# Kernel optimization log

Hardware: AMD Instinct MI355X
Metric: run time of the kernel (lower is better)

## Reference

```python
import jax, jax.numpy as jnp
import numpy as np

D_STATE = 16
D_CONV = 4
DT_RANK = 2  # ceil(d_model/16) with d_model=32


def _conv2d(x, w, b, pad, dil=1, groups=1):
    y = jax.lax.conv_general_dilated(
        x, w, (1, 1), ((pad, pad), (pad, pad)), rhs_dilation=(dil, dil),
        feature_group_count=groups, dimension_numbers=('NCHW', 'OIHW', 'NCHW'))
    return y + b[None, :, None, None]


def _ssm(xc, delta, A, Bc, Cc, D):
    # xc,delta: (B,L,Di); A: (Di,N); Bc,Cc: (B,L,N)
    dA = jnp.exp(delta[..., None] * A)                       # (B,L,Di,N)
    dBx = delta[..., None] * Bc[:, :, None, :] * xc[..., None]
    def comb(e1, e2):
        a1, b1 = e1
        a2, b2 = e2
        return a2 * a1, a2 * b1 + b2
    _, h = jax.lax.associative_scan(comb, (dA, dBx), axis=1)  # h_t = dA_t*h_{t-1}+dBx_t
    return jnp.einsum('bldn,bln->bld', h, Cc) + xc * D


def _dir(xin, cw, cb, wx, wdt, bdt, A_log, D):
    # causal depthwise conv1d over L, then silu
    L = xin.shape[1]
    xp = jnp.pad(xin, ((0, 0), (D_CONV - 1, 0), (0, 0)))
    xc = sum(xp[:, k:k + L, :] * cw[:, k] for k in range(D_CONV)) + cb
    xc = jax.nn.silu(xc)
    dbc = xc @ wx.T                                          # (B,L,dt_rank+2N)
    dt, Bc, Cc = jnp.split(dbc, [DT_RANK, DT_RANK + D_STATE], axis=-1)
    delta = jax.nn.softplus(dt @ wdt.T + bdt)
    return _ssm(xc, delta, -jnp.exp(A_log), Bc, Cc, D)


def _mamba(xn, w_in, cwf, cbf, wxf, wdtf, bdtf, Af, Df,
           cwb, cbb, wxb, wdtb, bdtb, Ab, Db, w_out):
    xz = xn @ w_in.T                                         # (B,L,2*Di)
    xin, z = jnp.split(xz, 2, axis=-1)
    y_f = _dir(xin, cwf, cbf, wxf, wdtf, bdtf, Af, Df)
    y_b = jnp.flip(_dir(jnp.flip(xin, axis=1), cwb, cbb, wxb, wdtb, bdtb, Ab, Db), axis=1)
    return ((y_f + y_b) * jax.nn.silu(z)) @ w_out.T          # bimamba v2: sum of directions


def _forward(x, w_att, b_att, ln_w, ln_b, w_in,
             conv_w_f, conv_b_f, wx_f, wdt_f, bdt_f, A_log_f, D_f,
             conv_w_b, conv_b_b, wx_b, wdt_b, bdt_b, A_log_b, D_b,
             w_out, w_se, b_se, w_conv, b_conv):
    B, C, H, W = x.shape
    att1 = x
    xa = _conv2d(x, w_att, b_att, pad=9, dil=3, groups=C)    # dilated depthwise, same HxW
    xf = xa.reshape(B, C, H * W).transpose(0, 2, 1)          # (B,L,C)
    mu = xf.mean(-1, keepdims=True)
    var = xf.var(-1, keepdims=True)
    xn = (xf - mu) / jnp.sqrt(var + 1e-5) * ln_w + ln_b
    out = _mamba(xn, w_in, conv_w_f, conv_b_f, wx_f, wdt_f, bdt_f, A_log_f, D_f,
                 conv_w_b, conv_b_b, wx_b, wdt_b, bdt_b, A_log_b, D_b, w_out)
    att2 = out.transpose(0, 2, 1).reshape(B, C, H, W)
    att = jnp.concatenate([att1, att2], axis=1)
    pooled = jnp.concatenate([att.mean(1, keepdims=True), att.max(1, keepdims=True)], axis=1)
    se = jax.nn.sigmoid(_conv2d(pooled, w_se, b_se, pad=3))
    output = att1 * se[:, 0:1] + att2 * se[:, 1:2]
    return _conv2d(output, w_conv, b_conv, pad=1)


def setup_inputs() -> dict:
    key = jax.random.key(0)
    ks = jax.random.split(key, 16)
    B, C, H, W = 4, 32, 96, 96
    Di, OUT = 64, 64
    n = jax.random.normal
    A_log = jnp.tile(jnp.log(jnp.arange(1, D_STATE + 1, dtype=jnp.float32)), (Di, 1))
    return {
        'x': n(ks[0], (B, C, H, W), jnp.float32),
        'w_att': n(ks[1], (C, 1, 7, 7), jnp.float32) * 0.05,
        'b_att': jnp.zeros((C,), jnp.float32),
        'ln_w': jnp.ones((C,), jnp.float32),
        'ln_b': jnp.zeros((C,), jnp.float32),
        'w_in': n(ks[2], (2 * Di, C), jnp.float32) / np.sqrt(C),
        'conv_w_f': n(ks[3], (Di, D_CONV), jnp.float32) * 0.3,
        'conv_b_f': jnp.zeros((Di,), jnp.float32),
        'wx_f': n(ks[4], (DT_RANK + 2 * D_STATE, Di), jnp.float32) / np.sqrt(Di),
        'wdt_f': n(ks[5], (Di, DT_RANK), jnp.float32) * 0.5,
        'bdt_f': n(ks[6], (Di,), jnp.float32) * 0.1,
        'A_log_f': A_log,
        'D_f': jnp.ones((Di,), jnp.float32),
        'conv_w_b': n(ks[7], (Di, D_CONV), jnp.float32) * 0.3,
        'conv_b_b': jnp.zeros((Di,), jnp.float32),
        'wx_b': n(ks[8], (DT_RANK + 2 * D_STATE, Di), jnp.float32) / np.sqrt(Di),
        'wdt_b': n(ks[9], (Di, DT_RANK), jnp.float32) * 0.5,
        'bdt_b': n(ks[10], (Di,), jnp.float32) * 0.1,
        'A_log_b': A_log,
        'D_b': jnp.ones((Di,), jnp.float32),
        'w_out': n(ks[11], (C, Di), jnp.float32) / np.sqrt(Di),
        'w_se': n(ks[12], (2, 2, 7, 7), jnp.float32) * 0.1,
        'b_se': jnp.zeros((2,), jnp.float32),
        'w_conv': n(ks[13], (OUT, C, 3, 3), jnp.float32) * 0.06,
        'b_conv': jnp.zeros((OUT,), jnp.float32),
    }


def reference(x, w_att, b_att, ln_w, ln_b, w_in,
              conv_w_f, conv_b_f, wx_f, wdt_f, bdt_f, A_log_f, D_f,
              conv_w_b, conv_b_b, wx_b, wdt_b, bdt_b, A_log_b, D_b,
              w_out, w_se, b_se, w_conv, b_conv):
    return _forward(x, w_att, b_att, ln_w, ln_b, w_in,
                    conv_w_f, conv_b_f, wx_f, wdt_f, bdt_f, A_log_f, D_f,
                    conv_w_b, conv_b_b, wx_b, wdt_b, bdt_b, A_log_b, D_b,
                    w_out, w_se, b_se, w_conv, b_conv)
```

## Files before the change

### kernel.cpp

```cpp
#include <hip/hip_runtime.h>
#include <math.h>

#define BB 4
#define CH 32
#define HH 96
#define WW 96
#define LL (HH*WW)
#define DI 64
#define NS 16
#define BL (BB*LL)
#define NCH 144
#define CLEN (LL/NCH)
#define GG 8

__device__ __forceinline__ float sigmoidf_(float x){ return 1.f/(1.f+__expf(-x)); }
__device__ __forceinline__ float siluf_(float x){ return x*sigmoidf_(x); }
__device__ __forceinline__ float softplusf_(float x){
  return (x > 15.f) ? x : __logf(1.f + __expf(x));
}
#define WAVE_LDS_FENCE() do { asm volatile("s_waitcnt lgkmcnt(0)" ::: "memory"); __builtin_amdgcn_sched_barrier(0); } while(0)

__global__ __launch_bounds__(256) void k1_conv_att(
    const float* __restrict__ x, const float* __restrict__ w,
    const float* __restrict__ bias, float* __restrict__ xa){
  int idx = blockIdx.x*256 + threadIdx.x;
  if (idx >= BB*CH*LL) return;
  int w0 = idx % WW; int h0 = (idx/WW) % HH; int c = (idx/LL) % CH;
  const float* xp = x + (idx/LL)*LL;
  const float* wp = w + c*49;
  float acc = bias[c];
  #pragma unroll
  for (int kh=0; kh<7; ++kh){
    int hh = h0 + 3*kh - 9;
    if ((unsigned)hh >= HH) continue;
    const float* row = xp + hh*WW;
    #pragma unroll
    for (int kw=0; kw<7; ++kw){
      int ww = w0 + 3*kw - 9;
      if ((unsigned)ww < WW) acc += row[ww]*wp[kh*7+kw];
    }
  }
  xa[idx] = acc;
}

__global__ __launch_bounds__(128) void k2_ln_inproj(
    const float* __restrict__ xa, const float* __restrict__ w_in,
    const float* __restrict__ ln_w, const float* __restrict__ ln_b,
    float* __restrict__ xin, float* __restrict__ zs){
  __shared__ float xs[CH*68];
  __shared__ float smu[64], srs[64];
  int tid = threadIdx.x;
  int tg0 = blockIdx.x*64;
  int bb = tg0 / LL;
  int l0 = tg0 % LL;
  const float* xab = xa + bb*CH*LL + l0;
  for (int r=0; r<16; ++r){
    int idx = r*128 + tid;
    int c = idx >> 6, t = idx & 63;
    xs[c*68+t] = xab[c*LL + t];
  }
  int j = tid;
  float wlj[CH];
  float swl=0.f, bj=0.f;
  #pragma unroll
  for (int c=0;c<CH;++c){
    float wv = ln_w[c]*w_in[j*CH+c];
    wlj[c] = wv; swl += wv;
    bj += ln_b[c]*w_in[j*CH+c];
  }
  __syncthreads();
  if (tid < 64){
    float s=0.f, s2=0.f;
    #pragma unroll
    for (int c=0;c<CH;++c){ float v = xs[c*68+tid]; s+=v; s2+=v*v; }
    float mu = s*(1.f/CH);
    float var = s2*(1.f/CH) - mu*mu;
    smu[tid]=mu; srs[tid]=rsqrtf(var+1e-5f);
  }
  __syncthreads();
  for (int t4=0;t4<16;++t4){
    float a0=0.f,a1=0.f,a2=0.f,a3=0.f;
    #pragma unroll
    for (int c=0;c<CH;++c){
      float4 xv = *(const float4*)&xs[c*68 + t4*4];
      float wv = wlj[c];
      a0 += xv.x*wv; a1 += xv.y*wv; a2 += xv.z*wv; a3 += xv.w*wv;
    }
    float av[4] = {a0,a1,a2,a3};
    #pragma unroll
    for (int q=0;q<4;++q){
      int t = t4*4+q;
      float out = srs[t]*(av[q] - smu[t]*swl) + bj;
      int base = ((bb*LL) + l0 + t)*DI;
      if (j < DI) xin[base + j] = out;
      else        zs[base + (j-DI)] = siluf_(out);
    }
  }
}

__global__ __launch_bounds__(64) void k3_fused(
    const float* __restrict__ xin,
    const float* __restrict__ cw_f, const float* __restrict__ cb_f,
    const float* __restrict__ wx_f, const float* __restrict__ wdt_f, const float* __restrict__ bdt_f,
    const float* __restrict__ Al_f,
    const float* __restrict__ cw_b, const float* __restrict__ cb_b,
    const float* __restrict__ wx_b, const float* __restrict__ wdt_b, const float* __restrict__ bdt_b,
    const float* __restrict__ Al_b,
    float* __restrict__ xc_f, float* __restrict__ dl_f, float* __restrict__ Bc_f, float* __restrict__ Cc_f,
    float* __restrict__ xc_b, float* __restrict__ dl_b, float* __restrict__ Bc_b, float* __restrict__ Cc_b,
    float* __restrict__ aggP, float* __restrict__ aggS){
  int lane = threadIdx.x;
  int dir = blockIdx.y;
  int bb = blockIdx.z;
  int ch = blockIdx.x;
  int p0 = ch*CLEN;
  const float* cw  = dir? cw_b : cw_f;
  const float* cb  = dir? cb_b : cb_f;
  const float* wx  = dir? wx_b : wx_f;
  const float* wdt = dir? wdt_b : wdt_f;
  const float* bdt = dir? bdt_b : bdt_f;
  const float* Al  = dir? Al_b : Al_f;
  float* xcbuf = dir? xc_b : xc_f;
  float* dlbuf = dir? dl_b : dl_f;
  float* Bcb   = dir? Bc_b : Bc_f;
  float* Ccb   = dir? Cc_b : Cc_f;

  __shared__ float xcs[GG*64];
  __shared__ float bcs[GG*16];
  __shared__ float dtb[GG*2];

  int d = lane;
  float c0=cw[d*4+0], c1=cw[d*4+1], c2=cw[d*4+2], c3=cw[d*4+3], cbv=cb[d];
  float wd0=wdt[d*2], wd1=wdt[d*2+1], bd=bdt[d];
  float A[NS];
  #pragma unroll
  for (int n4=0;n4<4;++n4){
    float4 av = *(const float4*)&Al[d*NS + n4*4];
    A[n4*4+0] = -__expf(av.x); A[n4*4+1] = -__expf(av.y);
    A[n4*4+2] = -__expf(av.z); A[n4*4+3] = -__expf(av.w);
  }
  float wreg[64];
  if (lane < 34){
    #pragma unroll
    for (int c4=0;c4<16;++c4){
      float4 wv = *(const float4*)&wx[lane*64 + c4*4];
      wreg[c4*4+0]=wv.x; wreg[c4*4+1]=wv.y; wreg[c4*4+2]=wv.z; wreg[c4*4+3]=wv.w;
    }
  }
  float P[NS], S[NS];
  #pragma unroll
  for (int n=0;n<NS;++n){ P[n]=1.f; S[n]=0.f; }
  float u1=0.f,u2=0.f,u3=0.f;
  #pragma unroll
  for (int k=1;k<=3;++k){
    int pos = p0 - k;
    float v = 0.f;
    if (pos >= 0){ int ls = dir? (LL-1-pos) : pos; v = xin[(bb*LL+ls)*DI + d]; }
    if(k==1) u1=v; else if(k==2) u2=v; else u3=v;
  }

  for (int g=0; g<CLEN/GG; ++g){
    int pbase = p0 + g*GG;
    float xcr[GG];
    #pragma unroll
    for (int j=0;j<GG;++j){
      int pos = pbase + j;
      int ls = dir? (LL-1-pos) : pos;
      float u0 = xin[(bb*LL+ls)*DI + d];
      float xc = siluf_(cbv + c0*u3 + c1*u2 + c2*u1 + c3*u0);
      u3=u2; u2=u1; u1=u0;
      xcr[j] = xc;
      xcs[j*64+d] = xc;
    }
    #pragma unroll
    for (int j=0;j<GG;++j) xcbuf[(bb*LL+pbase+j)*DI + d] = xcr[j];
    WAVE_LDS_FENCE();
    if (lane < 34){
      #pragma unroll
      for (int j=0;j<GG;++j){
        float acc = 0.f;
        #pragma unroll
        for (int c4=0;c4<16;++c4){
          float4 xv = *(const float4*)&xcs[j*64 + c4*4];
          acc += xv.x*wreg[c4*4+0] + xv.y*wreg[c4*4+1]
               + xv.z*wreg[c4*4+2] + xv.w*wreg[c4*4+3];
        }
        int tb = bb*LL + pbase + j;
        if (lane < 2){
          dtb[j*2+lane] = acc;
        } else if (lane < 18){
          Bcb[tb*NS + lane-2] = acc;
          bcs[j*16 + lane-2] = acc;
        } else {
          Ccb[tb*NS + lane-18] = acc;
        }
      }
    }
    WAVE_LDS_FENCE();
    #pragma unroll
    for (int j=0;j<GG;++j){
      int tb = bb*LL + pbase + j;
      float dlt = softplusf_(dtb[j*2]*wd0 + dtb[j*2+1]*wd1 + bd);
      dlbuf[tb*DI + d] = dlt;
      float dx = dlt*xcr[j];
      #pragma unroll
      for (int n4=0;n4<4;++n4){
        float4 bv = *(const float4*)&bcs[j*16 + n4*4];
        float bvv[4] = {bv.x,bv.y,bv.z,bv.w};
        #pragma unroll
        for (int q=0;q<4;++q){
          int n = n4*4+q;
          float dA = __expf(dlt*A[n]);
          P[n] *= dA;
          S[n] = dA*S[n] + dx*bvv[q];
        }
      }
    }
  }
  int bdd = (bb*2+dir)*DI + d;
  float* pp = aggP + (bdd*NCH + ch)*NS;
  float* sp = aggS + (bdd*NCH + ch)*NS;
  #pragma unroll
  for (int n4=0;n4<4;++n4){
    *(float4*)&pp[n4*4] = make_float4(P[n4*4+0],P[n4*4+1],P[n4*4+2],P[n4*4+3]);
    *(float4*)&sp[n4*4] = make_float4(S[n4*4+0],S[n4*4+1],S[n4*4+2],S[n4*4+3]);
  }
}

__global__ __launch_bounds__(256) void p2_scan_agg(
    const float* __restrict__ aggP, const float* __restrict__ aggS,
    float* __restrict__ hin){
  int t = blockIdx.x*256 + threadIdx.x;
  if (t >= BB*2*DI*NS) return;
  int bdd = t >> 4, n = t & 15;
  float h = 0.f;
  #pragma unroll 4
  for (int k=0;k<NCH;++k){
    int i = (bdd*NCH + k)*NS + n;
    float pv = aggP[i], sv = aggS[i];
    hin[i] = h;
    h = pv*h + sv;
  }
}

__global__ __launch_bounds__(64) void p3_scan_out(
    const float* __restrict__ dl_f, const float* __restrict__ xc_f,
    const float* __restrict__ Bc_f, const float* __restrict__ Cc_f,
    const float* __restrict__ dl_b, const float* __restrict__ xc_b,
    const float* __restrict__ Bc_b, const float* __restrict__ Cc_b,
    const float* __restrict__ Al_f, const float* __restrict__ D_f,
    const float* __restrict__ Al_b, const float* __restrict__ D_b,
    const float* __restrict__ hin, float* __restrict__ y_f, float* __restrict__ y_b){
  int lane = threadIdx.x;
  int dir = blockIdx.y >> 1;
  int dhalf = blockIdx.y & 1;
  int bb = blockIdx.z; int ch = blockIdx.x;
  int d = dhalf*32 + (lane & 31);
  int nb = (lane >> 5) * 8;
  const float* dl = dir? dl_b : dl_f;
  const float* xc = dir? xc_b : xc_f;
  const float* Bc = dir? Bc_b : Bc_f;
  const float* Cc = dir? Cc_b : Cc_f;
  const float* Al = dir? Al_b : Al_f;
  const float* Dv = dir? D_b : D_f;
  float* y = dir? y_b : y_f;
  float A[8];
  #pragma unroll
  for (int n4=0;n4<2;++n4){
    float4 av = *(const float4*)&Al[d*NS + nb + n4*4];
    A[n4*4+0] = -__expf(av.x); A[n4*4+1] = -__expf(av.y);
    A[n4*4+2] = -__expf(av.z); A[n4*4+3] = -__expf(av.w);
  }
  float Dd = Dv[d];
  int bdd = (bb*2+dir)*DI + d;
  const float* hp = hin + (bdd*NCH + ch)*NS + nb;
  float h[8];
  #pragma unroll
  for (int n4=0;n4<2;++n4){
    float4 hv = *(const float4*)&hp[n4*4];
    h[n4*4+0]=hv.x; h[n4*4+1]=hv.y; h[n4*4+2]=hv.z; h[n4*4+3]=hv.w;
  }
  int p0 = ch*CLEN;
  #pragma unroll 2
  for (int t=0;t<CLEN;++t){
    int tb = bb*LL + p0 + t;
    float dlt = dl[tb*DI+d];
    float xcv = xc[tb*DI+d];
    float dx = dlt*xcv;
    float4 bv0 = *(const float4*)&Bc[tb*NS + nb];
    float4 bv1 = *(const float4*)&Bc[tb*NS + nb + 4];
    float4 cv0 = *(const float4*)&Cc[tb*NS + nb];
    float4 cv1 = *(const float4*)&Cc[tb*NS + nb + 4];
    float bvv[8]={bv0.x,bv0.y,bv0.z,bv0.w,bv1.x,bv1.y,bv1.z,bv1.w};
    float cvv[8]={cv0.x,cv0.y,cv0.z,cv0.w,cv1.x,cv1.y,cv1.z,cv1.w};
    float pacc[4]={0.f,0.f,0.f,0.f};
    #pragma unroll
    for (int n=0;n<8;++n){
      float dA = __expf(dlt*A[n]);
      h[n] = dA*h[n] + dx*bvv[n];
      pacc[n&3] += h[n]*cvv[n];
    }
    float acc = (pacc[0]+pacc[1]) + (pacc[2]+pacc[3]);
    float other = __shfl_xor(acc, 32, 64);
    if (lane < 32) y[tb*DI + d] = xcv*Dd + acc + other;
  }
}

__global__ __launch_bounds__(256) void k4_outproj(
    const float* __restrict__ y_f, const float* __restrict__ y_b, const float* __restrict__ zs,
    const float* __restrict__ w_out, float* __restrict__ att2){
  __shared__ float gt[64*64];
  __shared__ float wol[32*65];
  __shared__ float ot[32*65];
  int tid = threadIdx.x;
  int tg0 = blockIdx.x*64;
  int bb = tg0/LL, l0 = tg0%LL;
  for (int r=0;r<8;++r){
    int idx = r*256+tid;
    wol[(idx>>6)*65 + (idx&63)] = w_out[idx];
  }
  for (int r=0;r<16;++r){
    int idx = r*256+tid;
    int tk = idx>>6, d = idx&63;
    int l = l0+tk;
    int tbf = (bb*LL + l)*DI + d;
    int tbb = (bb*LL + (LL-1-l))*DI + d;
    gt[idx] = (y_f[tbf] + y_b[tbb]) * zs[tbf];
  }
  __syncthreads();
  int c = tid & 31, tsl = tid >> 5;
  for (int tg=0; tg<8; ++tg){
    int tk = tg*8+tsl;
    float acc=0.f;
    #pragma unroll
    for (int d=0;d<DI;++d) acc += gt[tk*64+d]*wol[c*65+d];
    ot[c*65+tk] = acc;
  }
  __syncthreads();
  float* a2 = att2 + bb*CH*LL + l0;
  for (int r=0;r<8;++r){
    int idx = r*256+tid;
    int cc2 = idx>>6, t = idx&63;
    a2[cc2*LL + t] = ot[cc2*65+t];
  }
}

__global__ __launch_bounds__(256) void k5a_pool(
    const float* __restrict__ x, const float* __restrict__ att2, float* __restrict__ pooled){
  int idx = blockIdx.x*256+threadIdx.x;
  if (idx>=BL) return;
  int bb = idx/LL, l = idx%LL;
  const float* xp = x + bb*CH*LL + l;
  const float* ap = att2 + bb*CH*LL + l;
  float s=0.f, m=-INFINITY;
  for (int c=0;c<CH;++c){
    float v1 = xp[c*LL], v2 = ap[c*LL];
    s += v1+v2;
    m = fmaxf(m, fmaxf(v1,v2));
  }
  pooled[(bb*2+0)*LL + l] = s*(1.f/64.f);
  pooled[(bb*2+1)*LL + l] = m;
}

__global__ __launch_bounds__(256) void k5b_se_combine(
    const float* __restrict__ x, const float* __restrict__ att2,
    const float* __restrict__ pooled, const float* __restrict__ w_se,
    const float* __restrict__ b_se, float* __restrict__ outbuf){
  int idx = blockIdx.x*256+threadIdx.x;
  if (idx>=BL) return;
  int bb = idx/LL, l = idx%LL;
  int h0 = l/WW, w0 = l%WW;
  float a0 = b_se[0], a1 = b_se[1];
  #pragma unroll
  for (int i=0;i<2;++i){
    const float* pp = pooled + (bb*2+i)*LL;
    for (int kh=0;kh<7;++kh){
      int hh = h0+kh-3; if((unsigned)hh>=HH) continue;
      for (int kw=0;kw<7;++kw){
        int ww2 = w0+kw-3; if((unsigned)ww2>=WW) continue;
        float v = pp[hh*WW+ww2];
        a0 += v*w_se[(i*7+kh)*7+kw];
        a1 += v*w_se[((2+i)*7+kh)*7+kw];
      }
    }
  }
  float se0 = sigmoidf_(a0), se1 = sigmoidf_(a1);
  const float* xp = x + bb*CH*LL + l;
  const float* ap = att2 + bb*CH*LL + l;
  float* op = outbuf + bb*CH*LL + l;
  for (int c=0;c<CH;++c) op[c*LL] = xp[c*LL]*se0 + ap[c*LL]*se1;
}

__global__ __launch_bounds__(256) void k6_conv3x3(
    const float* __restrict__ inb, const float* __restrict__ wc,
    const float* __restrict__ bc, float* __restrict__ out){
  __shared__ float lds[CH*3*98];
  int tid = threadIdx.x;
  int h = blockIdx.x, cohalf = blockIdx.y, bb = blockIdx.z;
  const float* ib = inb + bb*CH*LL;
  for (int r=0; r<36; ++r){
    int idx = r*256+tid;
    int ci = idx/(3*96); int rr = (idx/96)%3; int ww2 = idx%96;
    int hh = h + rr - 1;
    float v = ((unsigned)hh < HH) ? ib[ci*LL + hh*WW + ww2] : 0.f;
    lds[(ci*3+rr)*98 + 1 + ww2] = v;
  }
  if (tid < 96){
    int ci = tid/3, rr = tid%3;
    lds[(ci*3+rr)*98 + 0]  = 0.f;
    lds[(ci*3+rr)*98 + 97] = 0.f;
  }
  __syncthreads();
  int coslot = tid >> 4, wslot = tid & 15;
  int co0 = cohalf*32 + coslot*2, wb = wslot*6;
  float acc[2][6];
  #pragma unroll
  for (int q=0;q<2;++q)
    #pragma unroll
    for (int j2=0;j2<6;++j2) acc[q][j2]=0.f;
  for (int ci=0; ci<CH; ++ci){
    float wt[2][9];
    #pragma unroll
    for (int q=0;q<2;++q){
      const float* wp = wc + ((co0+q)*CH + ci)*9;
      #pragma unroll
      for (int k=0;k<9;++k) wt[q][k] = wp[k];
    }
    #pragma unroll
    for (int kh=0;kh<3;++kh){
      const float* row = &lds[(ci*3+kh)*98 + wb];
      float s[8];
      #pragma unroll
      for (int t2=0;t2<8;++t2) s[t2] = row[t2];
      #pragma unroll
      for (int q=0;q<2;++q)
        #pragma unroll
        for (int kw=0;kw<3;++kw){
          float wv = wt[q][kh*3+kw];
          #pragma unroll
          for (int j2=0;j2<6;++j2) acc[q][j2] += s[j2+kw]*wv;
        }
    }
  }
  #pragma unroll
  for (int q=0;q<2;++q){
    int co = co0+q;
    float bv = bc[co];
    float* op = out + (bb*64 + co)*LL + h*WW + wb;
    #pragma unroll
    for (int j2=0;j2<6;++j2) op[j2] = acc[q][j2]+bv;
  }
}

extern "C" void kernel_launch(void* const* d_in, const int* in_sizes, int n_in,
                              void* d_out, int out_size, void* d_ws, size_t ws_size,
                              hipStream_t stream){
  const float* x     = (const float*)d_in[0];
  const float* w_att = (const float*)d_in[1];
  const float* b_att = (const float*)d_in[2];
  const float* ln_w  = (const float*)d_in[3];
  const float* ln_b  = (const float*)d_in[4];
  const float* w_in  = (const float*)d_in[5];
  const float* cw_f  = (const float*)d_in[6];
  const float* cb_f  = (const float*)d_in[7];
  const float* wx_f  = (const float*)d_in[8];
  const float* wdt_f = (const float*)d_in[9];
  const float* bdt_f = (const float*)d_in[10];
  const float* Al_f  = (const float*)d_in[11];
  const float* D_f   = (const float*)d_in[12];
  const float* cw_b  = (const float*)d_in[13];
  const float* cb_b  = (const float*)d_in[14];
  const float* wx_b  = (const float*)d_in[15];
  const float* wdt_b = (const float*)d_in[16];
  const float* bdt_b = (const float*)d_in[17];
  const float* Al_b  = (const float*)d_in[18];
  const float* D_b   = (const float*)d_in[19];
  const float* w_out = (const float*)d_in[20];
  const float* w_se  = (const float*)d_in[21];
  const float* b_se  = (const float*)d_in[22];
  const float* w_conv= (const float*)d_in[23];
  const float* b_conv= (const float*)d_in[24];

  float* ws = (float*)d_ws;
  float* xa     = ws + 0;
  float* att2   = ws + 0;
  float* xin    = ws + 1179648;
  float* hin    = ws + 1179648;
  float* outbuf = ws + 1179648;
  float* pooled = ws + 2359296;
  float* zs     = ws + 3538944;
  float* xc_f   = ws + 5898240;
  float* xc_b   = ws + 8257536;
  float* dl_f   = ws + 10616832;
  float* dl_b   = ws + 12976128;
  float* Bc_f   = ws + 15335424;
  float* Bc_b   = ws + 15925248;
  float* Cc_f   = ws + 16515072;
  float* Cc_b   = ws + 17104896;
  float* y_f    = ws + 17694720;
  float* y_b    = ws + 20054016;
  float* aggP   = ws + 22413312;
  float* aggS   = ws + 23592960;

  k1_conv_att<<<4608,256,0,stream>>>(x, w_att, b_att, xa);
  k2_ln_inproj<<<576,128,0,stream>>>(xa, w_in, ln_w, ln_b, xin, zs);
  k3_fused<<<dim3(NCH,2,BB),64,0,stream>>>(xin,
      cw_f,cb_f,wx_f,wdt_f,bdt_f,Al_f, cw_b,cb_b,wx_b,wdt_b,bdt_b,Al_b,
      xc_f,dl_f,Bc_f,Cc_f, xc_b,dl_b,Bc_b,Cc_b, aggP,aggS);
  p2_scan_agg<<<32,256,0,stream>>>(aggP,aggS,hin);
  p3_scan_out<<<dim3(NCH,4,BB),64,0,stream>>>(dl_f,xc_f,Bc_f,Cc_f, dl_b,xc_b,Bc_b,Cc_b,
      Al_f,D_f, Al_b,D_b, hin, y_f,y_b);
  k4_outproj<<<576,256,0,stream>>>(y_f,y_b,zs,w_out,att2);
  k5a_pool<<<144,256,0,stream>>>(x, att2, pooled);
  k5b_se_combine<<<144,256,0,stream>>>(x, att2, pooled, w_se, b_se, outbuf);
  k6_conv3x3<<<dim3(HH,2,BB),256,0,stream>>>(outbuf, w_conv, b_conv, (float*)d_out);
}
```

Baseline: 370.3 us.

## Double scan chunks, shrink tiles, and split pooling/SE work across threads

Doubles the number of SSM scan chunks so the chunked scan kernels launch more blocks. The per-chunk decay product is now computed once as exp(A*sum(delta)) instead of a running per-step multiply, which removes one multiply per state per step. The layer-norm/in-projection and out-projection kernels process 32 positions per block instead of 64, doubling their grid size. The pooling and SE-combine kernels now spread channels and conv taps across four thread groups per position, using shared-memory reductions. Workspace offsets are reshuffled and the aggregate buffers alias the y buffers, which relies on y being written only after the aggregates are consumed.

```diff
diff --git a/kernel.cpp b/kernel.cpp
--- a/kernel.cpp
+++ b/kernel.cpp
@@ -9,7 +9,7 @@
 #define DI 64
 #define NS 16
 #define BL (BB*LL)
-#define NCH 144
+#define NCH 288
 #define CLEN (LL/NCH)
 #define GG 8
 
@@ -47,17 +47,17 @@
     const float* __restrict__ xa, const float* __restrict__ w_in,
     const float* __restrict__ ln_w, const float* __restrict__ ln_b,
     float* __restrict__ xin, float* __restrict__ zs){
-  __shared__ float xs[CH*68];
-  __shared__ float smu[64], srs[64];
+  __shared__ float xs[CH*36];
+  __shared__ float smu[32], srs[32];
   int tid = threadIdx.x;
-  int tg0 = blockIdx.x*64;
+  int tg0 = blockIdx.x*32;
   int bb = tg0 / LL;
   int l0 = tg0 % LL;
   const float* xab = xa + bb*CH*LL + l0;
-  for (int r=0; r<16; ++r){
+  for (int r=0; r<8; ++r){
     int idx = r*128 + tid;
-    int c = idx >> 6, t = idx & 63;
-    xs[c*68+t] = xab[c*LL + t];
+    int c = idx >> 5, t = idx & 31;
+    xs[c*36+t] = xab[c*LL + t];
   }
   int j = tid;
   float wlj[CH];
@@ -69,20 +69,20 @@
     bj += ln_b[c]*w_in[j*CH+c];
   }
   __syncthreads();
-  if (tid < 64){
+  if (tid < 32){
     float s=0.f, s2=0.f;
     #pragma unroll
-    for (int c=0;c<CH;++c){ float v = xs[c*68+tid]; s+=v; s2+=v*v; }
+    for (int c=0;c<CH;++c){ float v = xs[c*36+tid]; s+=v; s2+=v*v; }
     float mu = s*(1.f/CH);
     float var = s2*(1.f/CH) - mu*mu;
     smu[tid]=mu; srs[tid]=rsqrtf(var+1e-5f);
   }
   __syncthreads();
-  for (int t4=0;t4<16;++t4){
+  for (int t4=0;t4<8;++t4){
     float a0=0.f,a1=0.f,a2=0.f,a3=0.f;
     #pragma unroll
     for (int c=0;c<CH;++c){
-      float4 xv = *(const float4*)&xs[c*68 + t4*4];
+      float4 xv = *(const float4*)&xs[c*36 + t4*4];
       float wv = wlj[c];
       a0 += xv.x*wv; a1 += xv.y*wv; a2 += xv.z*wv; a3 += xv.w*wv;
     }
@@ -147,9 +147,10 @@
       wreg[c4*4+0]=wv.x; wreg[c4*4+1]=wv.y; wreg[c4*4+2]=wv.z; wreg[c4*4+3]=wv.w;
     }
   }
-  float P[NS], S[NS];
-  #pragma unroll
-  for (int n=0;n<NS;++n){ P[n]=1.f; S[n]=0.f; }
+  float S[NS];
+  #pragma unroll
+  for (int n=0;n<NS;++n) S[n]=0.f;
+  float sdl = 0.f;
   float u1=0.f,u2=0.f,u3=0.f;
   #pragma unroll
   for (int k=1;k<=3;++k){
@@ -202,6 +203,7 @@
       int tb = bb*LL + pbase + j;
       float dlt = softplusf_(dtb[j*2]*wd0 + dtb[j*2+1]*wd1 + bd);
       dlbuf[tb*DI + d] = dlt;
+      sdl += dlt;
       float dx = dlt*xcr[j];
       #pragma unroll
       for (int n4=0;n4<4;++n4){
@@ -211,7 +213,6 @@
         for (int q=0;q<4;++q){
           int n = n4*4+q;
           float dA = __expf(dlt*A[n]);
-          P[n] *= dA;
           S[n] = dA*S[n] + dx*bvv[q];
         }
       }
@@ -222,7 +223,8 @@
   float* sp = aggS + (bdd*NCH + ch)*NS;
   #pragma unroll
   for (int n4=0;n4<4;++n4){
-    *(float4*)&pp[n4*4] = make_float4(P[n4*4+0],P[n4*4+1],P[n4*4+2],P[n4*4+3]);
+    *(float4*)&pp[n4*4] = make_float4(__expf(A[n4*4+0]*sdl),__expf(A[n4*4+1]*sdl),
+                                      __expf(A[n4*4+2]*sdl),__expf(A[n4*4+3]*sdl));
     *(float4*)&sp[n4*4] = make_float4(S[n4*4+0],S[n4*4+1],S[n4*4+2],S[n4*4+3]);
   }
 }
@@ -309,17 +311,17 @@
 __global__ __launch_bounds__(256) void k4_outproj(
     const float* __restrict__ y_f, const float* __restrict__ y_b, const float* __restrict__ zs,
     const float* __restrict__ w_out, float* __restrict__ att2){
-  __shared__ float gt[64*64];
+  __shared__ float gt[32*64];
   __shared__ float wol[32*65];
-  __shared__ float ot[32*65];
+  __shared__ float ot[32*33];
   int tid = threadIdx.x;
-  int tg0 = blockIdx.x*64;
+  int tg0 = blockIdx.x*32;
   int bb = tg0/LL, l0 = tg0%LL;
   for (int r=0;r<8;++r){
     int idx = r*256+tid;
     wol[(idx>>6)*65 + (idx&63)] = w_out[idx];
   }
-  for (int r=0;r<16;++r){
+  for (int r=0;r<8;++r){
     int idx = r*256+tid;
     int tk = idx>>6, d = idx&63;
     int l = l0+tk;
@@ -329,66 +331,92 @@
   }
   __syncthreads();
   int c = tid & 31, tsl = tid >> 5;
-  for (int tg=0; tg<8; ++tg){
+  for (int tg=0; tg<4; ++tg){
     int tk = tg*8+tsl;
     float acc=0.f;
     #pragma unroll
     for (int d=0;d<DI;++d) acc += gt[tk*64+d]*wol[c*65+d];
-    ot[c*65+tk] = acc;
+    ot[c*33+tk] = acc;
   }
   __syncthreads();
   float* a2 = att2 + bb*CH*LL + l0;
-  for (int r=0;r<8;++r){
+  for (int r=0;r<4;++r){
     int idx = r*256+tid;
-    int cc2 = idx>>6, t = idx&63;
-    a2[cc2*LL + t] = ot[cc2*65+t];
+    int cc2 = idx>>5, t = idx&31;
+    a2[cc2*LL + t] = ot[cc2*33+t];
   }
 }
 
 __global__ __launch_bounds__(256) void k5a_pool(
     const float* __restrict__ x, const float* __restrict__ att2, float* __restrict__ pooled){
-  int idx = blockIdx.x*256+threadIdx.x;
-  if (idx>=BL) return;
-  int bb = idx/LL, l = idx%LL;
+  __shared__ float ps[4][64], pm[4][64];
+  int tid = threadIdx.x;
+  int lq = tid & 63, q = tid >> 6;
+  int gl = blockIdx.x*64 + lq;
+  int bb = gl/LL, l = gl%LL;
   const float* xp = x + bb*CH*LL + l;
   const float* ap = att2 + bb*CH*LL + l;
   float s=0.f, m=-INFINITY;
-  for (int c=0;c<CH;++c){
+  #pragma unroll
+  for (int cc=0;cc<8;++cc){
+    int c = q*8+cc;
     float v1 = xp[c*LL], v2 = ap[c*LL];
     s += v1+v2;
     m = fmaxf(m, fmaxf(v1,v2));
   }
-  pooled[(bb*2+0)*LL + l] = s*(1.f/64.f);
-  pooled[(bb*2+1)*LL + l] = m;
+  ps[q][lq] = s; pm[q][lq] = m;
+  __syncthreads();
+  if (tid < 64){
+    int gl2 = blockIdx.x*64 + tid;
+    int bb2 = gl2/LL, l2 = gl2%LL;
+    float ss = (ps[0][tid]+ps[1][tid]) + (ps[2][tid]+ps[3][tid]);
+    float mm = fmaxf(fmaxf(pm[0][tid],pm[1][tid]), fmaxf(pm[2][tid],pm[3][tid]));
+    pooled[(bb2*2+0)*LL + l2] = ss*(1.f/64.f);
+    pooled[(bb2*2+1)*LL + l2] = mm;
+  }
 }
 
 __global__ __launch_bounds__(256) void k5b_se_combine(
     const float* __restrict__ x, const float* __restrict__ att2,
     const float* __restrict__ pooled, const float* __restrict__ w_se,
     const float* __restrict__ b_se, float* __restrict__ outbuf){
-  int idx = blockIdx.x*256+threadIdx.x;
-  if (idx>=BL) return;
-  int bb = idx/LL, l = idx%LL;
+  __shared__ float pb[4][64];
+  __shared__ float sep[2][64];
+  int tid = threadIdx.x;
+  int lq = tid & 63, q = tid >> 6;
+  int i = q & 1, o = q >> 1;
+  int gl = blockIdx.x*64 + lq;
+  int bb = gl/LL, l = gl%LL;
   int h0 = l/WW, w0 = l%WW;
-  float a0 = b_se[0], a1 = b_se[1];
-  #pragma unroll
-  for (int i=0;i<2;++i){
-    const float* pp = pooled + (bb*2+i)*LL;
-    for (int kh=0;kh<7;++kh){
-      int hh = h0+kh-3; if((unsigned)hh>=HH) continue;
-      for (int kw=0;kw<7;++kw){
-        int ww2 = w0+kw-3; if((unsigned)ww2>=WW) continue;
-        float v = pp[hh*WW+ww2];
-        a0 += v*w_se[(i*7+kh)*7+kw];
-        a1 += v*w_se[((2+i)*7+kh)*7+kw];
-      }
-    }
-  }
-  float se0 = sigmoidf_(a0), se1 = sigmoidf_(a1);
+  const float* pp = pooled + (bb*2+i)*LL;
+  const float* wp = w_se + (o*2+i)*49;
+  float a = 0.f;
+  #pragma unroll
+  for (int kh=0;kh<7;++kh){
+    int hh = h0+kh-3; if((unsigned)hh>=HH) continue;
+    const float* row = pp + hh*WW;
+    #pragma unroll
+    for (int kw=0;kw<7;++kw){
+      int ww2 = w0+kw-3;
+      if((unsigned)ww2<WW) a += row[ww2]*wp[kh*7+kw];
+    }
+  }
+  pb[q][lq] = a;
+  __syncthreads();
+  if (tid < 128){
+    int oo = tid >> 6, l2 = tid & 63;
+    sep[oo][l2] = sigmoidf_(b_se[oo] + pb[oo*2+0][l2] + pb[oo*2+1][l2]);
+  }
+  __syncthreads();
+  float se0 = sep[0][lq], se1 = sep[1][lq];
   const float* xp = x + bb*CH*LL + l;
   const float* ap = att2 + bb*CH*LL + l;
   float* op = outbuf + bb*CH*LL + l;
-  for (int c=0;c<CH;++c) op[c*LL] = xp[c*LL]*se0 + ap[c*LL]*se1;
+  #pragma unroll
+  for (int cc=0;cc<8;++cc){
+    int c = q*8+cc;
+    op[c*LL] = xp[c*LL]*se0 + ap[c*LL]*se1;
+  }
 }
 
 __global__ __launch_bounds__(256) void k6_conv3x3(
@@ -487,31 +515,31 @@
   float* xin    = ws + 1179648;
   float* hin    = ws + 1179648;
   float* outbuf = ws + 1179648;
-  float* pooled = ws + 2359296;
-  float* zs     = ws + 3538944;
-  float* xc_f   = ws + 5898240;
-  float* xc_b   = ws + 8257536;
-  float* dl_f   = ws + 10616832;
-  float* dl_b   = ws + 12976128;
-  float* Bc_f   = ws + 15335424;
-  float* Bc_b   = ws + 15925248;
-  float* Cc_f   = ws + 16515072;
-  float* Cc_b   = ws + 17104896;
-  float* y_f    = ws + 17694720;
-  float* y_b    = ws + 20054016;
-  float* aggP   = ws + 22413312;
-  float* aggS   = ws + 23592960;
+  float* pooled = ws + 3538944;
+  float* zs     = ws + 3612672;
+  float* xc_f   = ws + 5971968;
+  float* xc_b   = ws + 8331264;
+  float* dl_f   = ws + 10690560;
+  float* dl_b   = ws + 13049856;
+  float* Bc_f   = ws + 15409152;
+  float* Bc_b   = ws + 15998976;
+  float* Cc_f   = ws + 16588800;
+  float* Cc_b   = ws + 17178624;
+  float* y_f    = ws + 17768448;
+  float* y_b    = ws + 20127744;
+  float* aggP   = y_f;
+  float* aggS   = y_b;
 
   k1_conv_att<<<4608,256,0,stream>>>(x, w_att, b_att, xa);
-  k2_ln_inproj<<<576,128,0,stream>>>(xa, w_in, ln_w, ln_b, xin, zs);
+  k2_ln_inproj<<<1152,128,0,stream>>>(xa, w_in, ln_w, ln_b, xin, zs);
   k3_fused<<<dim3(NCH,2,BB),64,0,stream>>>(xin,
       cw_f,cb_f,wx_f,wdt_f,bdt_f,Al_f, cw_b,cb_b,wx_b,wdt_b,bdt_b,Al_b,
       xc_f,dl_f,Bc_f,Cc_f, xc_b,dl_b,Bc_b,Cc_b, aggP,aggS);
   p2_scan_agg<<<32,256,0,stream>>>(aggP,aggS,hin);
   p3_scan_out<<<dim3(NCH,4,BB),64,0,stream>>>(dl_f,xc_f,Bc_f,Cc_f, dl_b,xc_b,Bc_b,Cc_b,
       Al_f,D_f, Al_b,D_b, hin, y_f,y_b);
-  k4_outproj<<<576,256,0,stream>>>(y_f,y_b,zs,w_out,att2);
-  k5a_pool<<<144,256,0,stream>>>(x, att2, pooled);
-  k5b_se_combine<<<144,256,0,stream>>>(x, att2, pooled, w_se, b_se, outbuf);
+  k4_outproj<<<1152,256,0,stream>>>(y_f,y_b,zs,w_out,att2);
+  k5a_pool<<<576,256,0,stream>>>(x, att2, pooled);
+  k5b_se_combine<<<576,256,0,stream>>>(x, att2, pooled, w_se, b_se, outbuf);
   k6_conv3x3<<<dim3(HH,2,BB),256,0,stream>>>(outbuf, w_conv, b_conv, (float*)d_out);
 }
```

Result: faster. 325.0 us (-12.2%).
